# Optimization experiments

Hardware: AMD Instinct MI355X
Metric: run time of the kernel (lower is better)

Reference implementation:

```python
import jax, jax.numpy as jnp
import numpy as np

WS = 7          # window size
HEADS = 8
SHIFT = WS // 2  # shift=True -> 3
C = 256
KD = C // HEADS  # key_dim = 32
LN_EPS = 1e-3    # keras LayerNormalization default


def setup_inputs() -> dict:
    key = jax.random.key(0)
    ks = jax.random.split(key, 12)
    s = 1.0 / np.sqrt(C)
    x = jax.random.normal(ks[0], (16, 112, 112, C), dtype=jnp.float32)
    wq = jax.random.normal(ks[1], (C, HEADS, KD), dtype=jnp.float32) * s
    bq = jnp.zeros((HEADS, KD), dtype=jnp.float32)
    wk = jax.random.normal(ks[2], (C, HEADS, KD), dtype=jnp.float32) * s
    bk = jnp.zeros((HEADS, KD), dtype=jnp.float32)
    wv = jax.random.normal(ks[3], (C, HEADS, KD), dtype=jnp.float32) * s
    bv = jnp.zeros((HEADS, KD), dtype=jnp.float32)
    wo = jax.random.normal(ks[4], (HEADS, KD, C), dtype=jnp.float32) * s
    bo = jnp.zeros((C,), dtype=jnp.float32)
    gamma = jnp.ones((C,), dtype=jnp.float32)
    beta = jnp.zeros((C,), dtype=jnp.float32)
    return {"x": x, "wq": wq, "bq": bq, "wk": wk, "bk": bk,
            "wv": wv, "bv": bv, "wo": wo, "bo": bo,
            "gamma": gamma, "beta": beta}


def _swin_window_attn(x, wq, bq, wk, bk, wv, bv, wo, bo, gamma, beta):
    b, h, w, c = x.shape
    pad_h = (WS - h % WS) % WS
    pad_w = (WS - w % WS) % WS
    if pad_h or pad_w:
        x = jnp.pad(x, ((0, 0), (0, pad_h), (0, pad_w), (0, 0)))
    hp, wp = h + pad_h, w + pad_w
    if SHIFT > 0:
        x = jnp.roll(x, shift=(-SHIFT, -SHIFT), axis=(1, 2))
    nh, nw = hp // WS, wp // WS
    # window partition: (b, nh, WS, nw, WS, c) -> (b*nh*nw, WS*WS, c)
    win = x.reshape(b, nh, WS, nw, WS, c).transpose(0, 1, 3, 2, 4, 5)
    win = win.reshape(b * nh * nw, WS * WS, c)
    # multi-head attention (keras MHA: query scaled by 1/sqrt(key_dim))
    q = jnp.einsum("nsc,chd->nshd", win, wq) + bq
    k = jnp.einsum("nsc,chd->nshd", win, wk) + bk
    v = jnp.einsum("nsc,chd->nshd", win, wv) + bv
    scores = jnp.einsum("nqhd,nkhd->nhqk", q, k) / jnp.sqrt(jnp.float32(KD)).astype(q.dtype)
    probs = jax.nn.softmax(scores, axis=-1)
    ctx = jnp.einsum("nhqk,nkhd->nqhd", probs, v)
    attn = jnp.einsum("nqhd,hdc->nqc", ctx, wo) + bo
    # residual + LayerNorm
    y = attn + win
    mu = jnp.mean(y, axis=-1, keepdims=True)
    var = jnp.mean(jnp.square(y - mu), axis=-1, keepdims=True)
    y = (y - mu) * jax.lax.rsqrt(var + LN_EPS) * gamma + beta
    # window reverse
    out = y.reshape(b, nh, nw, WS, WS, c).transpose(0, 1, 3, 2, 4, 5)
    out = out.reshape(b, hp, wp, c)
    if SHIFT > 0:
        out = jnp.roll(out, shift=(SHIFT, SHIFT), axis=(1, 2))
    if pad_h or pad_w:
        out = out[:, :h, :w, :]
    return out


def reference(x, wq, bq, wk, bk, wv, bv, wo, bo, gamma, beta):
    return _swin_window_attn(x, wq, bq, wk, bk, wv, bv, wo, bo, gamma, beta)
```

## Files before the change

### kernel.cpp

```cpp
#include <hip/hip_runtime.h>
#include <hip/hip_bf16.h>

typedef __attribute__((ext_vector_type(8))) short short8;
typedef __attribute__((ext_vector_type(4))) short short4v;
typedef __attribute__((ext_vector_type(4))) float float4v;
typedef __attribute__((ext_vector_type(2))) unsigned int uint2v;

#define LDS_BYTES 144384
#define XBF_OFF   0
#define VT_OFF    33792
#define Q_OFF     70656
#define K_OFF     104448
#define P_OFF     70656
#define CTX_OFF   33792
#define Y_OFF     70656

__device__ __forceinline__ unsigned short f2bf_rn(float f) {
    union { __hip_bfloat16 b; unsigned short u; } v;
    v.b = __float2bfloat16(f);
    return v.u;
}
__device__ __forceinline__ unsigned int pk2bf(float a, float b) {
    union { __hip_bfloat162 h; unsigned int u; } v;
    v.h = __float22bfloat162_rn(make_float2(a, b));
    return v.u;
}
__device__ __forceinline__ float bf2f(unsigned short h) {
    union { unsigned int u; float f; } v; v.u = ((unsigned int)h) << 16;
    return v.f;
}

__global__ void prep_weights(const float* __restrict__ wq, const float* __restrict__ wk,
                             const float* __restrict__ wv, const float* __restrict__ wo,
                             unsigned short* __restrict__ wfrag) {
    int tid = blockIdx.x * 256 + threadIdx.x;
    if (tid >= 4 * 65536) return;
    int m = tid >> 16;
    int e = tid & 65535;
    int j = e & 7;
    int lane = (e >> 3) & 63;
    int nt2 = (e >> 9) & 15;
    int ks = e >> 13;
    int c = ks * 32 + (lane >> 4) * 8 + j;
    int o = nt2 * 16 + (lane & 15);
    const float* W = (m == 0) ? wq : (m == 1) ? wk : (m == 2) ? wv : wo;
    wfrag[tid] = f2bf_rn(W[c * 256 + o]);
}

__global__ __launch_bounds__(1024, 4) void swin_fused(
    const float* __restrict__ x,
    const unsigned short* __restrict__ wfrag,
    const float* __restrict__ bq, const float* __restrict__ bk,
    const float* __restrict__ bv, const float* __restrict__ bo,
    const float* __restrict__ gamma, const float* __restrict__ beta,
    float* __restrict__ out)
{
    extern __shared__ char smem[];
    const int tid = threadIdx.x;
    const int w    = tid >> 6;
    const int h    = w & 7;
    const int half = w >> 3;
    const int l   = tid & 63;
    const int l15 = l & 15;
    const int l4  = l >> 4;
    const int nt2 = 2 * h + half;

    const int blk = blockIdx.x;
    const int bb  = blk >> 8;
    const int wh  = (blk >> 4) & 15;
    const int ww  = blk & 15;

    unsigned short* Xbf = (unsigned short*)(smem + XBF_OFF);

    for (int idx = tid; idx < 64 * 64; idx += 1024) {
        const int tok = idx >> 6;
        const int c4  = idx & 63;
        float4v f = (float4v){0.f, 0.f, 0.f, 0.f};
        if (tok < 49) {
            const int i = tok / 7;
            const int j = tok - 7 * i;
            int gr = wh * 7 + i + 3; if (gr >= 112) gr -= 112;
            int gc = ww * 7 + j + 3; if (gc >= 112) gc -= 112;
            f = *(const float4v*)(x + (((size_t)bb * 112 + gr) * 112 + gc) * 256 + c4 * 4);
        }
        uint2v u;
        u.x = pk2bf(f.x, f.y);
        u.y = pk2bf(f.z, f.w);
        *(uint2v*)(Xbf + tok * 264 + c4 * 4) = u;
    }
    __syncthreads();

    unsigned short* Qs = (unsigned short*)(smem + Q_OFF);
    unsigned short* Ks = (unsigned short*)(smem + K_OFF);
    unsigned short* Vt = (unsigned short*)(smem + VT_OFF);

    {
        float4v accQ[4], accK[4], accV[4];
#pragma unroll
        for (int mt = 0; mt < 4; ++mt) {
            accQ[mt] = (float4v){0.f, 0.f, 0.f, 0.f};
            accK[mt] = (float4v){0.f, 0.f, 0.f, 0.f};
            accV[mt] = (float4v){0.f, 0.f, 0.f, 0.f};
        }
        const unsigned short* wqf = wfrag;
        const unsigned short* wkf = wfrag + 65536;
        const unsigned short* wvf = wfrag + 2 * 65536;
#pragma unroll
        for (int ks = 0; ks < 8; ++ks) {
            const int woff = ((ks * 16 + nt2) * 64 + l) * 8;
            short8 bq_ = *(const short8*)(wqf + woff);
            short8 bk_ = *(const short8*)(wkf + woff);
            short8 bv_ = *(const short8*)(wvf + woff);
            short8 afr[4];
#pragma unroll
            for (int mt = 0; mt < 4; ++mt)
                afr[mt] = *(const short8*)(Xbf + (mt * 16 + l15) * 264 + ks * 32 + l4 * 8);
            __builtin_amdgcn_s_setprio(1);
#pragma unroll
            for (int mt = 0; mt < 4; ++mt)
                accQ[mt] = __builtin_amdgcn_mfma_f32_16x16x32_bf16(afr[mt], bq_, accQ[mt], 0, 0, 0);
#pragma unroll
            for (int mt = 0; mt < 4; ++mt)
                accK[mt] = __builtin_amdgcn_mfma_f32_16x16x32_bf16(afr[mt], bk_, accK[mt], 0, 0, 0);
#pragma unroll
            for (int mt = 0; mt < 4; ++mt)
                accV[mt] = __builtin_amdgcn_mfma_f32_16x16x32_bf16(afr[mt], bv_, accV[mt], 0, 0, 0);
            __builtin_amdgcn_s_setprio(0);
        }
        const int o = nt2 * 16 + l15;
        const float biasq = bq[o];
        const float biask = bk[o];
        const float biasv = bv[o];
#pragma unroll
        for (int mt = 0; mt < 4; ++mt) {
            const int tok0 = mt * 16 + l4 * 4;
#pragma unroll
            for (int r = 0; r < 4; ++r) {
                Qs[(tok0 + r) * 264 + o] = f2bf_rn(accQ[mt][r] + biasq);
                Ks[(tok0 + r) * 264 + o] = f2bf_rn(accK[mt][r] + biask);
            }
        }
        const int d = half * 16 + l15;
#pragma unroll
        for (int mt = 0; mt < 4; ++mt) {
            uint2v u;
            u.x = pk2bf(accV[mt][0] + biasv, accV[mt][1] + biasv);
            u.y = pk2bf(accV[mt][2] + biasv, accV[mt][3] + biasv);
            *(uint2v*)(Vt + h * 2304 + d * 72 + mt * 16 + l4 * 4) = u;
        }
    }
    __syncthreads();

    float4v sa[4][2];
#pragma unroll
    for (int mt = 0; mt < 4; ++mt)
#pragma unroll
        for (int nt = 0; nt < 2; ++nt)
            sa[mt][nt] = (float4v){0.f, 0.f, 0.f, 0.f};
    {
        short8 kfr[4], qfr[2];
#pragma unroll
        for (int mt = 0; mt < 4; ++mt)
            kfr[mt] = *(const short8*)(Ks + (mt * 16 + l15) * 264 + 32 * h + l4 * 8);
#pragma unroll
        for (int nt = 0; nt < 2; ++nt)
            qfr[nt] = *(const short8*)(Qs + (32 * half + nt * 16 + l15) * 264 + 32 * h + l4 * 8);
        __builtin_amdgcn_s_setprio(1);
#pragma unroll
        for (int mt = 0; mt < 4; ++mt)
#pragma unroll
            for (int nt = 0; nt < 2; ++nt)
                sa[mt][nt] = __builtin_amdgcn_mfma_f32_16x16x32_bf16(kfr[mt], qfr[nt], sa[mt][nt], 0, 0, 0);
        __builtin_amdgcn_s_setprio(0);
    }
    __syncthreads();

    unsigned short* Ph = (unsigned short*)(smem + P_OFF) + h * 4608;
    const float SCALE = 0.17677669529663687f;
#pragma unroll
    for (int nt = 0; nt < 2; ++nt) {
        float sv[4][4];
        float mx = -1e30f;
#pragma unroll
        for (int mt = 0; mt < 4; ++mt)
#pragma unroll
            for (int r = 0; r < 4; ++r) {
                const bool valid = (mt < 3) || ((l4 == 0) && (r == 0));
                sv[mt][r] = valid ? sa[mt][nt][r] * SCALE : -1e30f;
                mx = fmaxf(mx, sv[mt][r]);
            }
        mx = fmaxf(mx, __shfl_xor(mx, 16, 64));
        mx = fmaxf(mx, __shfl_xor(mx, 32, 64));
        float p[4][4];
        float sum = 0.f;
#pragma unroll
        for (int mt = 0; mt < 4; ++mt)
#pragma unroll
            for (int r = 0; r < 4; ++r) {
                p[mt][r] = __expf(sv[mt][r] - mx);
                sum += p[mt][r];
            }
        sum += __shfl_xor(sum, 16, 64);
        sum += __shfl_xor(sum, 32, 64);
        const float inv = 1.f / sum;
        const int q = 32 * half + nt * 16 + l15;
#pragma unroll
        for (int mt = 0; mt < 4; ++mt) {
            uint2v u;
            u.x = pk2bf(p[mt][0] * inv, p[mt][1] * inv);
            u.y = pk2bf(p[mt][2] * inv, p[mt][3] * inv);
            *(uint2v*)(Ph + q * 72 + mt * 16 + l4 * 4) = u;
        }
    }

    float4v ca[2][2];
#pragma unroll
    for (int mtl = 0; mtl < 2; ++mtl)
#pragma unroll
        for (int nt = 0; nt < 2; ++nt)
            ca[mtl][nt] = (float4v){0.f, 0.f, 0.f, 0.f};
#pragma unroll
    for (int ks = 0; ks < 2; ++ks) {
        short8 afr[2];
#pragma unroll
        for (int mtl = 0; mtl < 2; ++mtl)
            afr[mtl] = *(const short8*)(Ph + (32 * half + mtl * 16 + l15) * 72 + ks * 32 + l4 * 8);
        __builtin_amdgcn_s_setprio(1);
#pragma unroll
        for (int nt = 0; nt < 2; ++nt) {
            short8 bfr = *(const short8*)(Vt + h * 2304 + (nt * 16 + l15) * 72 + ks * 32 + l4 * 8);
#pragma unroll
            for (int mtl = 0; mtl < 2; ++mtl)
                ca[mtl][nt] = __builtin_amdgcn_mfma_f32_16x16x32_bf16(afr[mtl], bfr, ca[mtl][nt], 0, 0, 0);
        }
        __builtin_amdgcn_s_setprio(0);
    }
    __syncthreads();

    unsigned short* Ctx = (unsigned short*)(smem + CTX_OFF);
#pragma unroll
    for (int nt = 0; nt < 2; ++nt) {
        const int o = 32 * h + nt * 16 + l15;
#pragma unroll
        for (int mtl = 0; mtl < 2; ++mtl) {
            const int tok0 = (2 * half + mtl) * 16 + l4 * 4;
            Ctx[(tok0 + 0) * 264 + o] = f2bf_rn(ca[mtl][nt][0]);
            Ctx[(tok0 + 1) * 264 + o] = f2bf_rn(ca[mtl][nt][1]);
            Ctx[(tok0 + 2) * 264 + o] = f2bf_rn(ca[mtl][nt][2]);
            Ctx[(tok0 + 3) * 264 + o] = f2bf_rn(ca[mtl][nt][3]);
        }
    }
    __syncthreads();

    float4v oa[4];
#pragma unroll
    for (int mt = 0; mt < 4; ++mt) oa[mt] = (float4v){0.f, 0.f, 0.f, 0.f};
    const unsigned short* womat = wfrag + 3 * 65536;
#pragma unroll
    for (int ks = 0; ks < 8; ++ks) {
        short8 bfr = *(const short8*)(womat + ((ks * 16 + nt2) * 64 + l) * 8);
        short8 afr[4];
#pragma unroll
        for (int mt = 0; mt < 4; ++mt)
            afr[mt] = *(const short8*)(Ctx + (mt * 16 + l15) * 264 + ks * 32 + l4 * 8);
        __builtin_amdgcn_s_setprio(1);
#pragma unroll
        for (int mt = 0; mt < 4; ++mt)
            oa[mt] = __builtin_amdgcn_mfma_f32_16x16x32_bf16(afr[mt], bfr, oa[mt], 0, 0, 0);
        __builtin_amdgcn_s_setprio(0);
    }
    float* Y = (float*)(smem + Y_OFF);
    {
        const int cout = nt2 * 16 + l15;
        const float bias = bo[cout];
#pragma unroll
        for (int mt = 0; mt < 4; ++mt)
#pragma unroll
            for (int r = 0; r < 4; ++r) {
                const int tok = mt * 16 + l4 * 4 + r;
                Y[tok * 260 + cout] = oa[mt][r] + bias;
            }
    }
    __syncthreads();

    const float4v g4  = *(const float4v*)(gamma + l * 4);
    const float4v be4 = *(const float4v*)(beta + l * 4);
#pragma unroll
    for (int t = 0; t < 4; ++t) {
        const int tok = w + t * 16;
        if (tok < 49) {
            float4v f = *(const float4v*)(Y + tok * 260 + l * 4);
            short4v xr = *(const short4v*)(Xbf + tok * 264 + l * 4);
            f.x += bf2f((unsigned short)xr.x);
            f.y += bf2f((unsigned short)xr.y);
            f.z += bf2f((unsigned short)xr.z);
            f.w += bf2f((unsigned short)xr.w);
            float sum = f.x + f.y + f.z + f.w;
            float sq  = f.x * f.x + f.y * f.y + f.z * f.z + f.w * f.w;
#pragma unroll
            for (int msk = 1; msk < 64; msk <<= 1) {
                sum += __shfl_xor(sum, msk, 64);
                sq  += __shfl_xor(sq,  msk, 64);
            }
            const float mu   = sum * (1.f / 256.f);
            const float var  = sq * (1.f / 256.f) - mu * mu;
            const float rstd = rsqrtf(var + 1e-3f);
            const int i = tok / 7;
            const int j = tok - 7 * i;
            int gr = wh * 7 + i + 3; if (gr >= 112) gr -= 112;
            int gc = ww * 7 + j + 3; if (gc >= 112) gc -= 112;
            float4v o4;
            o4.x = (f.x - mu) * rstd * g4.x + be4.x;
            o4.y = (f.y - mu) * rstd * g4.y + be4.y;
            o4.z = (f.z - mu) * rstd * g4.z + be4.z;
            o4.w = (f.w - mu) * rstd * g4.w + be4.w;
            *(float4v*)(out + (((size_t)bb * 112 + gr) * 112 + gc) * 256 + l * 4) = o4;
        }
    }
}

extern "C" void kernel_launch(void* const* d_in, const int* in_sizes, int n_in,
                              void* d_out, int out_size, void* d_ws, size_t ws_size,
                              hipStream_t stream) {
    const float* x     = (const float*)d_in[0];
    const float* wq    = (const float*)d_in[1];
    const float* bq    = (const float*)d_in[2];
    const float* wk    = (const float*)d_in[3];
    const float* bk    = (const float*)d_in[4];
    const float* wv    = (const float*)d_in[5];
    const float* bv    = (const float*)d_in[6];
    const float* wo    = (const float*)d_in[7];
    const float* bo    = (const float*)d_in[8];
    const float* gamma = (const float*)d_in[9];
    const float* beta  = (const float*)d_in[10];
    float* out = (float*)d_out;
    unsigned short* wfrag = (unsigned short*)d_ws;

    prep_weights<<<1024, 256, 0, stream>>>(wq, wk, wv, wo, wfrag);

    hipFuncSetAttribute((const void*)swin_fused,
                        hipFuncAttributeMaxDynamicSharedMemorySize, LDS_BYTES);
    swin_fused<<<4096, 1024, LDS_BYTES, stream>>>(x, wfrag, bq, bk, bv, bo, gamma, beta, out);
}
```

Before: 277.6 us.

## Keep softmax probabilities in registers as MFMA operands; restructure LayerNorm reduction

Softmax probabilities are packed straight into bf16 MFMA A-operand registers instead of being written to LDS and read back. This removes a __syncthreads and the P buffer, shrinking the LDS footprint. V fragments are now gathered with two 8-byte reads to match the new k-ordering of the register layout. The LayerNorm epilogue is also reorganised so 16 lanes share one token, each handling 16 channels, which cuts the cross-lane shuffle chain from 6 steps to 4, though the global stores become less coalesced per instruction.

```diff
diff --git a/kernel.cpp b/kernel.cpp
--- a/kernel.cpp
+++ b/kernel.cpp
@@ -6,12 +6,11 @@
 typedef __attribute__((ext_vector_type(4))) float float4v;
 typedef __attribute__((ext_vector_type(2))) unsigned int uint2v;
 
-#define LDS_BYTES 144384
+#define LDS_BYTES 138240
 #define XBF_OFF   0
 #define VT_OFF    33792
 #define Q_OFF     70656
 #define K_OFF     104448
-#define P_OFF     70656
 #define CTX_OFF   33792
 #define Y_OFF     70656
 
@@ -29,6 +28,7 @@
     union { unsigned int u; float f; } v; v.u = ((unsigned int)h) << 16;
     return v.f;
 }
+union U8 { unsigned int u[4]; short8 s; };
 
 __global__ void prep_weights(const float* __restrict__ wq, const float* __restrict__ wk,
                              const float* __restrict__ wv, const float* __restrict__ wo,
@@ -173,9 +173,8 @@
                 sa[mt][nt] = __builtin_amdgcn_mfma_f32_16x16x32_bf16(kfr[mt], qfr[nt], sa[mt][nt], 0, 0, 0);
         __builtin_amdgcn_s_setprio(0);
     }
-    __syncthreads();
-
-    unsigned short* Ph = (unsigned short*)(smem + P_OFF) + h * 4608;
+
+    short8 pa[2][2];
     const float SCALE = 0.17677669529663687f;
 #pragma unroll
     for (int nt = 0; nt < 2; ++nt) {
@@ -203,14 +202,17 @@
         sum += __shfl_xor(sum, 16, 64);
         sum += __shfl_xor(sum, 32, 64);
         const float inv = 1.f / sum;
-        const int q = 32 * half + nt * 16 + l15;
-#pragma unroll
-        for (int mt = 0; mt < 4; ++mt) {
-            uint2v u;
-            u.x = pk2bf(p[mt][0] * inv, p[mt][1] * inv);
-            u.y = pk2bf(p[mt][2] * inv, p[mt][3] * inv);
-            *(uint2v*)(Ph + q * 72 + mt * 16 + l4 * 4) = u;
-        }
+        U8 t0, t1;
+        t0.u[0] = pk2bf(p[0][0] * inv, p[0][1] * inv);
+        t0.u[1] = pk2bf(p[0][2] * inv, p[0][3] * inv);
+        t0.u[2] = pk2bf(p[1][0] * inv, p[1][1] * inv);
+        t0.u[3] = pk2bf(p[1][2] * inv, p[1][3] * inv);
+        t1.u[0] = pk2bf(p[2][0] * inv, p[2][1] * inv);
+        t1.u[1] = pk2bf(p[2][2] * inv, p[2][3] * inv);
+        t1.u[2] = pk2bf(p[3][0] * inv, p[3][1] * inv);
+        t1.u[3] = pk2bf(p[3][2] * inv, p[3][3] * inv);
+        pa[nt][0] = t0.s;
+        pa[nt][1] = t1.s;
     }
 
     float4v ca[2][2];
@@ -221,19 +223,18 @@
             ca[mtl][nt] = (float4v){0.f, 0.f, 0.f, 0.f};
 #pragma unroll
     for (int ks = 0; ks < 2; ++ks) {
-        short8 afr[2];
-#pragma unroll
-        for (int mtl = 0; mtl < 2; ++mtl)
-            afr[mtl] = *(const short8*)(Ph + (32 * half + mtl * 16 + l15) * 72 + ks * 32 + l4 * 8);
-        __builtin_amdgcn_s_setprio(1);
-#pragma unroll
-        for (int nt = 0; nt < 2; ++nt) {
-            short8 bfr = *(const short8*)(Vt + h * 2304 + (nt * 16 + l15) * 72 + ks * 32 + l4 * 8);
+#pragma unroll
+        for (int ntv = 0; ntv < 2; ++ntv) {
+            const unsigned short* vrow = Vt + h * 2304 + (ntv * 16 + l15) * 72 + ks * 32 + l4 * 4;
+            uint2v lo = *(const uint2v*)(vrow);
+            uint2v hi = *(const uint2v*)(vrow + 16);
+            U8 b; b.u[0] = lo.x; b.u[1] = lo.y; b.u[2] = hi.x; b.u[3] = hi.y;
+            __builtin_amdgcn_s_setprio(1);
 #pragma unroll
             for (int mtl = 0; mtl < 2; ++mtl)
-                ca[mtl][nt] = __builtin_amdgcn_mfma_f32_16x16x32_bf16(afr[mtl], bfr, ca[mtl][nt], 0, 0, 0);
-        }
-        __builtin_amdgcn_s_setprio(0);
+                ca[mtl][ntv] = __builtin_amdgcn_mfma_f32_16x16x32_bf16(pa[mtl][ks], b.s, ca[mtl][ntv], 0, 0, 0);
+            __builtin_amdgcn_s_setprio(0);
+        }
     }
     __syncthreads();
 
@@ -283,38 +284,57 @@
     }
     __syncthreads();
 
-    const float4v g4  = *(const float4v*)(gamma + l * 4);
-    const float4v be4 = *(const float4v*)(beta + l * 4);
-#pragma unroll
-    for (int t = 0; t < 4; ++t) {
-        const int tok = w + t * 16;
-        if (tok < 49) {
-            float4v f = *(const float4v*)(Y + tok * 260 + l * 4);
-            short4v xr = *(const short4v*)(Xbf + tok * 264 + l * 4);
-            f.x += bf2f((unsigned short)xr.x);
-            f.y += bf2f((unsigned short)xr.y);
-            f.z += bf2f((unsigned short)xr.z);
-            f.w += bf2f((unsigned short)xr.w);
-            float sum = f.x + f.y + f.z + f.w;
-            float sq  = f.x * f.x + f.y * f.y + f.z * f.z + f.w * f.w;
-#pragma unroll
-            for (int msk = 1; msk < 64; msk <<= 1) {
-                sum += __shfl_xor(sum, msk, 64);
-                sq  += __shfl_xor(sq,  msk, 64);
-            }
+    {
+        const int tq = 4 * w + l4;
+        const int c0 = l15 * 16;
+        float4v y[4];
+        if (tq < 49) {
+#pragma unroll
+            for (int k = 0; k < 4; ++k)
+                y[k] = *(const float4v*)(Y + tq * 260 + c0 + 4 * k);
+            short8 xr0 = *(const short8*)(Xbf + tq * 264 + c0);
+            short8 xr1 = *(const short8*)(Xbf + tq * 264 + c0 + 8);
+#pragma unroll
+            for (int e = 0; e < 4; ++e) {
+                y[0][e] += bf2f((unsigned short)xr0[e]);
+                y[1][e] += bf2f((unsigned short)xr0[e + 4]);
+                y[2][e] += bf2f((unsigned short)xr1[e]);
+                y[3][e] += bf2f((unsigned short)xr1[e + 4]);
+            }
+        } else {
+#pragma unroll
+            for (int k = 0; k < 4; ++k) y[k] = (float4v){0.f, 0.f, 0.f, 0.f};
+        }
+        float sum = 0.f, sq = 0.f;
+#pragma unroll
+        for (int k = 0; k < 4; ++k)
+#pragma unroll
+            for (int e = 0; e < 4; ++e) { sum += y[k][e]; sq += y[k][e] * y[k][e]; }
+#pragma unroll
+        for (int msk = 1; msk < 16; msk <<= 1) {
+            sum += __shfl_xor(sum, msk, 64);
+            sq  += __shfl_xor(sq,  msk, 64);
+        }
+        if (tq < 49) {
             const float mu   = sum * (1.f / 256.f);
             const float var  = sq * (1.f / 256.f) - mu * mu;
             const float rstd = rsqrtf(var + 1e-3f);
-            const int i = tok / 7;
-            const int j = tok - 7 * i;
+            const int i = tq / 7;
+            const int j = tq - 7 * i;
             int gr = wh * 7 + i + 3; if (gr >= 112) gr -= 112;
             int gc = ww * 7 + j + 3; if (gc >= 112) gc -= 112;
-            float4v o4;
-            o4.x = (f.x - mu) * rstd * g4.x + be4.x;
-            o4.y = (f.y - mu) * rstd * g4.y + be4.y;
-            o4.z = (f.z - mu) * rstd * g4.z + be4.z;
-            o4.w = (f.w - mu) * rstd * g4.w + be4.w;
-            *(float4v*)(out + (((size_t)bb * 112 + gr) * 112 + gc) * 256 + l * 4) = o4;
+            float* op = out + (((size_t)bb * 112 + gr) * 112 + gc) * 256 + c0;
+#pragma unroll
+            for (int k = 0; k < 4; ++k) {
+                const float4v g4  = *(const float4v*)(gamma + c0 + 4 * k);
+                const float4v be4 = *(const float4v*)(beta  + c0 + 4 * k);
+                float4v o4;
+                o4.x = (y[k].x - mu) * rstd * g4.x + be4.x;
+                o4.y = (y[k].y - mu) * rstd * g4.y + be4.y;
+                o4.z = (y[k].z - mu) * rstd * g4.z + be4.z;
+                o4.w = (y[k].w - mu) * rstd * g4.w + be4.w;
+                *(float4v*)(op + 4 * k) = o4;
+            }
         }
     }
 }
```

New measurement: 310.0 us. 1.12x slower.

## Keep softmax probabilities in registers as MFMA operands instead of LDS

Applied to the files above, without the earlier changes.

The softmax output is packed straight into bf16 register fragments and fed to the P·V MFMA, so the probability round trip through LDS and one __syncthreads are removed. V^T is now stored with a permuted token layout so its k-ordering matches the register-resident P fragments. This shrinks the LDS footprint, which may allow more blocks per CU. The risk is that the permuted ordering is wrong and gives incorrect results, and the extra live registers may raise register pressure.

```diff
diff --git a/kernel.cpp b/kernel.cpp
--- a/kernel.cpp
+++ b/kernel.cpp
@@ -6,12 +6,11 @@
 typedef __attribute__((ext_vector_type(4))) float float4v;
 typedef __attribute__((ext_vector_type(2))) unsigned int uint2v;
 
-#define LDS_BYTES 144384
+#define LDS_BYTES 138240
 #define XBF_OFF   0
 #define VT_OFF    33792
 #define Q_OFF     70656
 #define K_OFF     104448
-#define P_OFF     70656
 #define CTX_OFF   33792
 #define Y_OFF     70656
 
@@ -29,6 +28,7 @@
     union { unsigned int u; float f; } v; v.u = ((unsigned int)h) << 16;
     return v.f;
 }
+union U8 { unsigned int u[4]; short8 s; };
 
 __global__ void prep_weights(const float* __restrict__ wq, const float* __restrict__ wk,
                              const float* __restrict__ wv, const float* __restrict__ wo,
@@ -146,7 +146,7 @@
             uint2v u;
             u.x = pk2bf(accV[mt][0] + biasv, accV[mt][1] + biasv);
             u.y = pk2bf(accV[mt][2] + biasv, accV[mt][3] + biasv);
-            *(uint2v*)(Vt + h * 2304 + d * 72 + mt * 16 + l4 * 4) = u;
+            *(uint2v*)(Vt + h * 2304 + d * 72 + 32 * (mt >> 1) + 8 * l4 + 4 * (mt & 1)) = u;
         }
     }
     __syncthreads();
@@ -173,9 +173,8 @@
                 sa[mt][nt] = __builtin_amdgcn_mfma_f32_16x16x32_bf16(kfr[mt], qfr[nt], sa[mt][nt], 0, 0, 0);
         __builtin_amdgcn_s_setprio(0);
     }
-    __syncthreads();
-
-    unsigned short* Ph = (unsigned short*)(smem + P_OFF) + h * 4608;
+
+    short8 pa[2][2];
     const float SCALE = 0.17677669529663687f;
 #pragma unroll
     for (int nt = 0; nt < 2; ++nt) {
@@ -203,14 +202,17 @@
         sum += __shfl_xor(sum, 16, 64);
         sum += __shfl_xor(sum, 32, 64);
         const float inv = 1.f / sum;
-        const int q = 32 * half + nt * 16 + l15;
-#pragma unroll
-        for (int mt = 0; mt < 4; ++mt) {
-            uint2v u;
-            u.x = pk2bf(p[mt][0] * inv, p[mt][1] * inv);
-            u.y = pk2bf(p[mt][2] * inv, p[mt][3] * inv);
-            *(uint2v*)(Ph + q * 72 + mt * 16 + l4 * 4) = u;
-        }
+        U8 t0, t1;
+        t0.u[0] = pk2bf(p[0][0] * inv, p[0][1] * inv);
+        t0.u[1] = pk2bf(p[0][2] * inv, p[0][3] * inv);
+        t0.u[2] = pk2bf(p[1][0] * inv, p[1][1] * inv);
+        t0.u[3] = pk2bf(p[1][2] * inv, p[1][3] * inv);
+        t1.u[0] = pk2bf(p[2][0] * inv, p[2][1] * inv);
+        t1.u[1] = pk2bf(p[2][2] * inv, p[2][3] * inv);
+        t1.u[2] = pk2bf(p[3][0] * inv, p[3][1] * inv);
+        t1.u[3] = pk2bf(p[3][2] * inv, p[3][3] * inv);
+        pa[nt][0] = t0.s;
+        pa[nt][1] = t1.s;
     }
 
     float4v ca[2][2];
@@ -221,19 +223,15 @@
             ca[mtl][nt] = (float4v){0.f, 0.f, 0.f, 0.f};
 #pragma unroll
     for (int ks = 0; ks < 2; ++ks) {
-        short8 afr[2];
-#pragma unroll
-        for (int mtl = 0; mtl < 2; ++mtl)
-            afr[mtl] = *(const short8*)(Ph + (32 * half + mtl * 16 + l15) * 72 + ks * 32 + l4 * 8);
-        __builtin_amdgcn_s_setprio(1);
-#pragma unroll
-        for (int nt = 0; nt < 2; ++nt) {
-            short8 bfr = *(const short8*)(Vt + h * 2304 + (nt * 16 + l15) * 72 + ks * 32 + l4 * 8);
+#pragma unroll
+        for (int ntv = 0; ntv < 2; ++ntv) {
+            short8 bfr = *(const short8*)(Vt + h * 2304 + (ntv * 16 + l15) * 72 + ks * 32 + l4 * 8);
+            __builtin_amdgcn_s_setprio(1);
 #pragma unroll
             for (int mtl = 0; mtl < 2; ++mtl)
-                ca[mtl][nt] = __builtin_amdgcn_mfma_f32_16x16x32_bf16(afr[mtl], bfr, ca[mtl][nt], 0, 0, 0);
-        }
-        __builtin_amdgcn_s_setprio(0);
+                ca[mtl][ntv] = __builtin_amdgcn_mfma_f32_16x16x32_bf16(pa[mtl][ks], bfr, ca[mtl][ntv], 0, 0, 0);
+            __builtin_amdgcn_s_setprio(0);
+        }
     }
     __syncthreads();
 
```

New measurement: 272.3 us. Within noise of the previous version (-1.9%).
